# Kernel optimization log

Measured on AMD Instinct MI355X. Metric: run time of the kernel, lower is better.

Reference implementation:

```python
import jax, jax.numpy as jnp
import numpy as np

DIM = 1024
HEADS = 16
HEAD_DIM = 64
INNER = HEADS * HEAD_DIM
SCALE = HEAD_DIM ** -0.5


def setup_inputs() -> dict:
    key = jax.random.key(0)
    k1, k2, k3, k4 = jax.random.split(key, 4)
    x = jax.random.normal(k1, (4, 2048, DIM), dtype=jnp.float32)
    # nn.Linear(dim, 3*inner) without bias; weight stored [out, in], we keep [in, out]
    w_qkv = jax.random.normal(k2, (DIM, 3 * INNER), dtype=jnp.float32) * (DIM ** -0.5)
    w_proj = jax.random.normal(k3, (INNER, DIM), dtype=jnp.float32) * (INNER ** -0.5)
    b_proj = jax.random.normal(k4, (DIM,), dtype=jnp.float32) * 0.01
    return {"x": x, "w_qkv": w_qkv, "w_proj": w_proj, "b_proj": b_proj}


def reference(x, w_qkv, w_proj, b_proj):
    B, N, _ = x.shape
    qkv = x @ w_qkv                                   # [B,N,3*inner]
    qkv = qkv.reshape(B, N, 3, HEADS, HEAD_DIM)
    q = qkv[:, :, 0].transpose(0, 2, 1, 3)           # [B,H,N,D]
    k = qkv[:, :, 1].transpose(0, 2, 1, 3)
    v = qkv[:, :, 2].transpose(0, 2, 1, 3)
    attn = jnp.einsum("bhqd,bhkd->bhqk", q, k) * SCALE
    attn = jax.nn.softmax(attn, axis=-1)
    out = jnp.einsum("bhqk,bhkd->bhqd", attn, v)     # [B,H,N,D]
    out = out.transpose(0, 2, 1, 3).reshape(B, N, INNER)
    return out @ w_proj + b_proj
```

## Files before the change

### kernel.cpp

```cpp
#include <hip/hip_runtime.h>

typedef unsigned short u16;
typedef unsigned int   u32;
typedef __attribute__((ext_vector_type(2))) float    f32x2;
typedef __attribute__((ext_vector_type(4))) float    f32x4;
typedef __attribute__((ext_vector_type(8))) __bf16   bf16x8;
typedef __attribute__((ext_vector_type(8))) unsigned short u16x8;
typedef __attribute__((ext_vector_type(4))) unsigned short u16x4;
typedef __attribute__((ext_vector_type(4))) float    float4v;

#define MFMA16(a,b,c) __builtin_amdgcn_mfma_f32_16x16x32_bf16((a),(b),(c),0,0,0)
#define QSCALE 0.18033688011112042f

__device__ __forceinline__ u16 f2b(float f){
  union { float f; unsigned u; } v; v.f = f;
  return (u16)((v.u + 0x7fffu + ((v.u >> 16) & 1u)) >> 16);
}

__device__ __forceinline__ u32 cvt_pk_bf16(float lo, float hi){
  u32 r;
  asm("v_cvt_pk_bf16_f32 %0, %1, %2" : "=v"(r) : "v"(lo), "v"(hi));
  return r;
}

__device__ __forceinline__ float exp2_raw(float x){
  float r;
  asm("v_exp_f32 %0, %1" : "=v"(r) : "v"(x));
  return r;
}

__device__ __forceinline__ f32x2 lo2(f32x4 v){ return __builtin_shufflevector(v, v, 0, 1); }
__device__ __forceinline__ f32x2 hi2(f32x4 v){ return __builtin_shufflevector(v, v, 2, 3); }

__device__ __forceinline__ void gload_lds16(const void* g, void* l){
  __builtin_amdgcn_global_load_lds(
      (const __attribute__((address_space(1))) void*)g,
      (__attribute__((address_space(3))) void*)l, 16, 0, 0);
}

__global__ void cast_f32_bf16(const float* __restrict__ in, u16* __restrict__ out, int n4){
  int i = blockIdx.x * blockDim.x + threadIdx.x;
  int st = gridDim.x * blockDim.x;
  for (; i < n4; i += st){
    float4v v = ((const float4v*)in)[i];
    u16x4 o;
    o[0] = f2b(v[0]); o[1] = f2b(v[1]); o[2] = f2b(v[2]); o[3] = f2b(v[3]);
    ((u16x4*)out)[i] = o;
  }
}

__global__ void tcast(const float* __restrict__ src, u16* __restrict__ dst, int R, int C){
  __shared__ float tile[32][33];
  int tx = threadIdx.x, ty = threadIdx.y;
  int c0 = blockIdx.x * 32, r0 = blockIdx.y * 32;
  #pragma unroll
  for (int i = 0; i < 4; i++)
    tile[ty + i*8][tx] = src[(long)(r0 + ty + i*8) * C + c0 + tx];
  __syncthreads();
  #pragma unroll
  for (int i = 0; i < 4; i++)
    dst[(long)(c0 + ty + i*8) * R + r0 + tx] = f2b(tile[tx][ty + i*8]);
}

template<int MODE>
__global__ __launch_bounds__(512, 2) void gemm8(
    const u16* __restrict__ A, const u16* __restrict__ Bt,
    int M, int N, int K,
    float* __restrict__ outF, const float* __restrict__ bias,
    u16* __restrict__ qb, u16* __restrict__ kb, u16* __restrict__ vtb)
{
  extern __shared__ u16 lds[];
  u16* aL = lds;
  u16* bL = lds + 49152;

  const int t  = threadIdx.x;
  const int l  = t & 63, lr = l & 15, lg = l >> 4;
  const int w  = t >> 6;
  const int wm = w >> 2, wn = w & 3;
  const long mbase = (long)blockIdx.x * 256;
  const long nbase = (long)blockIdx.y * 128;

  const int xr0 = t >> 3;
  const int xc  = t & 7;
  const int xswz = (xc ^ (xr0 & 7)) << 3;

#define STG(F_) do { \
    const int T_ = (F_) >> 2, h_ = (F_) & 3, slot_ = T_ % 3; \
    if ((h_ & 1) == 0){ const int ah = h_ >> 1; \
      const u16* g_ = A + (mbase + ah*128 + xr0)*(long)K + T_*64 + xswz; \
      u16* d_ = aL + slot_*16384 + ah*8192 + t*8; \
      gload_lds16(g_, d_); \
      gload_lds16(g_ + 64*(long)K, d_ + 4096); \
    } else { const int bh_ = h_ >> 1; \
      const u16* g_ = Bt + (nbase + bh_*64 + xr0)*(long)K + T_*64 + xswz; \
      gload_lds16(g_, bL + slot_*8192 + bh_*4096 + t*8); } \
  } while(0)

#define VMCNT(n) asm volatile("s_waitcnt vmcnt(" #n ")" ::: "memory")
#define BAR() __builtin_amdgcn_s_barrier()

  f32x4 z = {0.f,0.f,0.f,0.f};
  f32x4 acc[8][2];
  #pragma unroll
  for (int a = 0; a < 8; a++){ acc[a][0] = z; acc[a][1] = z; }

  STG(0); STG(1); STG(2); STG(3);
  STG(4); STG(5); STG(6); STG(7);
  VMCNT(6);
  BAR();

  for (int T = 0; T < 16; ++T){
    const int abuf = (T % 3) * 16384;
    const int bbuf = (T % 3) * 8192;
    bf16x8 af[8], bf[2];

    #pragma unroll
    for (int i = 0; i < 8; i++){
      const int ra = wm*128 + i*16 + lr;
      af[i] = *(const bf16x8*)&aL[abuf + ra*64 + ((lg^(ra&7))<<3)];
    }
    #pragma unroll
    for (int j = 0; j < 2; j++){
      const int rb = wn*32 + j*16 + lr;
      bf[j] = *(const bf16x8*)&bL[bbuf + rb*64 + ((lg^(rb&7))<<3)];
    }
    if (T < 14){ STG(4*(T+2)); STG(4*(T+2)+1); }
    __builtin_amdgcn_s_setprio(1);
    #pragma unroll
    for (int i = 0; i < 8; i++){
      acc[i][0] = MFMA16(af[i], bf[0], acc[i][0]);
      acc[i][1] = MFMA16(af[i], bf[1], acc[i][1]);
    }
    __builtin_amdgcn_s_setprio(0);
    BAR();

    #pragma unroll
    for (int i = 0; i < 8; i++){
      const int ra = wm*128 + i*16 + lr;
      af[i] = *(const bf16x8*)&aL[abuf + ra*64 + (((4+lg)^(ra&7))<<3)];
    }
    #pragma unroll
    for (int j = 0; j < 2; j++){
      const int rb = wn*32 + j*16 + lr;
      bf[j] = *(const bf16x8*)&bL[bbuf + rb*64 + (((4+lg)^(rb&7))<<3)];
    }
    if (T < 14){ STG(4*(T+2)+2); STG(4*(T+2)+3); }
    if (T < 14){ VMCNT(6); } else if (T == 14){ VMCNT(0); }
    BAR();
    __builtin_amdgcn_s_setprio(1);
    #pragma unroll
    for (int i = 0; i < 8; i++){
      acc[i][0] = MFMA16(af[i], bf[0], acc[i][0]);
      acc[i][1] = MFMA16(af[i], bf[1], acc[i][1]);
    }
    __builtin_amdgcn_s_setprio(0);
    BAR();
  }
#undef STG
#undef VMCNT
#undef BAR

  if (MODE == 0){
    #pragma unroll
    for (int a = 0; a < 8; a++){
      #pragma unroll
      for (int j = 0; j < 2; j++){
        int col   = (int)nbase + wn*32 + j*16 + lr;
        int which = col >> 10;
        int h     = (col >> 6) & 15;
        int d     = col & 63;
        int m0    = (int)mbase + wm*128 + a*16 + lg*4;
        int b     = m0 >> 11, ns0 = m0 & 2047;
        int bh    = (b << 4) + h;
        if (which == 2){
          u16x4 pk;
          #pragma unroll
          for (int r = 0; r < 4; r++) pk[r] = f2b(acc[a][j][r]);
          *(u16x4*)&vtb[((long)bh*64 + d)*2048 + ns0] = pk;
        } else {
          u16* dst  = (which == 0) ? qb : kb;
          float scl = (which == 0) ? QSCALE : 1.0f;
          #pragma unroll
          for (int r = 0; r < 4; r++)
            dst[((long)bh * 2048 + ns0 + r) * 64 + d] = f2b(acc[a][j][r] * scl);
        }
      }
    }
  } else {
    #pragma unroll
    for (int a = 0; a < 8; a++){
      #pragma unroll
      for (int j = 0; j < 2; j++){
        int c = (int)nbase + wn*32 + j*16 + lr;
        float bv = bias[c];
        #pragma unroll
        for (int r = 0; r < 4; r++){
          int m = (int)mbase + wm*128 + a*16 + lg*4 + r;
          outF[(long)m * N + c] = acc[a][j][r] + bv;
        }
      }
    }
  }
}

__global__ __launch_bounds__(256, 2) void attn_fused(
    const u16* __restrict__ qb, const u16* __restrict__ kb,
    const u16* __restrict__ vtb, u16* __restrict__ ob)
{
  __shared__ u16 k_lds[2][64*64];
  __shared__ u16 vt_lds[2][64*64];
  const int t  = threadIdx.x;
  const int l  = t & 63, lr = l & 15, lg = l >> 4;
  const int w  = t >> 6;
  const int bid = blockIdx.x;
  const int vid = (bid & 7) * 128 + (bid >> 3);
  const int bh = vid >> 4, qt = vid & 15;
  const int qrow = qt*128 + w*32;
  const int h7 = lr & 7;

  const u16* Qp = qb + ((long)bh*2048 + qrow)*64;
  bf16x8 qfA0 = *(const bf16x8*)&Qp[lr*64 + lg*8];
  bf16x8 qfA1 = *(const bf16x8*)&Qp[lr*64 + 32 + lg*8];
  bf16x8 qfB0 = *(const bf16x8*)&Qp[(16+lr)*64 + lg*8];
  bf16x8 qfB1 = *(const bf16x8*)&Qp[(16+lr)*64 + 32 + lg*8];

  const int r1 = t >> 3;
  const int cx = ((t & 7) ^ (r1 & 7)) * 8;
  const u16* Kp = kb  + (long)bh*2048*64;
  const u16* Vt = vtb + (long)bh*64*2048;
  const int koff0 = r1*64 + cx,        koff1 = (r1+32)*64 + cx;
  const int voff0 = r1*2048 + cx,      voff1 = (r1+32)*2048 + cx;

#define STAGE(kv, buf) do { \
    gload_lds16(Kp + (long)(kv)*64 + koff0, &k_lds[buf][t*8]); \
    gload_lds16(Kp + (long)(kv)*64 + koff1, &k_lds[buf][2048 + t*8]); \
    gload_lds16(Vt + (kv) + voff0, &vt_lds[buf][t*8]); \
    gload_lds16(Vt + (kv) + voff1, &vt_lds[buf][2048 + t*8]); \
  } while(0)

  f32x4 z = {0.f,0.f,0.f,0.f};
  f32x4 oaccA[4] = {z,z,z,z}, oaccB[4] = {z,z,z,z};
  f32x2 sAacc = {0.f, 0.f}, sBacc = {0.f, 0.f};

  STAGE(0, 0);
  #pragma unroll 2
  for (int it = 0; it < 32; ++it){
    const int cur = it & 1;
    __syncthreads();
    if (it < 31) STAGE((it+1)*64, cur^1);

    const u16* kl = k_lds[cur];
    const u16* vl = vt_lds[cur];

    f32x4 stA[4], stB[4];
    __builtin_amdgcn_s_setprio(1);
    #pragma unroll
    for (int k4 = 0; k4 < 4; k4++){
      const int row = (k4*16 + lr)*64;
      bf16x8 kf0 = *(const bf16x8*)&kl[row + ((0+lg)^h7)*8];
      bf16x8 kf1 = *(const bf16x8*)&kl[row + ((4+lg)^h7)*8];
      stA[k4] = MFMA16(kf0, qfA0, z);
      stA[k4] = MFMA16(kf1, qfA1, stA[k4]);
      stB[k4] = MFMA16(kf0, qfB0, z);
      stB[k4] = MFMA16(kf1, qfB1, stB[k4]);
    }
    __builtin_amdgcn_s_setprio(0);

    u32 wvA[4][2], wvB[4][2];
    #pragma unroll
    for (int k4 = 0; k4 < 4; k4++){
      f32x2 e0 = lo2(stA[k4]), e1 = hi2(stA[k4]);
      e0[0] = exp2_raw(e0[0]); e0[1] = exp2_raw(e0[1]);
      e1[0] = exp2_raw(e1[0]); e1[1] = exp2_raw(e1[1]);
      sAacc += e0 + e1;
      wvA[k4][0] = cvt_pk_bf16(e0[0], e0[1]);
      wvA[k4][1] = cvt_pk_bf16(e1[0], e1[1]);
      f32x2 f0 = lo2(stB[k4]), f1 = hi2(stB[k4]);
      f0[0] = exp2_raw(f0[0]); f0[1] = exp2_raw(f0[1]);
      f1[0] = exp2_raw(f1[0]); f1[1] = exp2_raw(f1[1]);
      sBacc += f0 + f1;
      wvB[k4][0] = cvt_pk_bf16(f0[0], f0[1]);
      wvB[k4][1] = cvt_pk_bf16(f1[0], f1[1]);
    }

    union { u32 u[4]; bf16x8 v; } paA0, paA1, paB0, paB1;
    paA0.u[0]=wvA[0][0]; paA0.u[1]=wvA[0][1]; paA0.u[2]=wvA[1][0]; paA0.u[3]=wvA[1][1];
    paA1.u[0]=wvA[2][0]; paA1.u[1]=wvA[2][1]; paA1.u[2]=wvA[3][0]; paA1.u[3]=wvA[3][1];
    paB0.u[0]=wvB[0][0]; paB0.u[1]=wvB[0][1]; paB0.u[2]=wvB[1][0]; paB0.u[3]=wvB[1][1];
    paB1.u[0]=wvB[2][0]; paB1.u[1]=wvB[2][1]; paB1.u[2]=wvB[3][0]; paB1.u[3]=wvB[3][1];

    const int vhalf = (lg & 1) * 4;
    const int cA    = lg >> 1;
    #pragma unroll
    for (int nt = 0; nt < 4; nt++){
      const int rb = (nt*16 + lr)*64;
      u16x4 a0_ = *(const u16x4*)&vl[rb + ((cA     ^ h7)*8) + vhalf];
      u16x4 a1_ = *(const u16x4*)&vl[rb + (((cA+2) ^ h7)*8) + vhalf];
      u16x4 a2_ = *(const u16x4*)&vl[rb + (((cA+4) ^ h7)*8) + vhalf];
      u16x4 a3_ = *(const u16x4*)&vl[rb + (((cA+6) ^ h7)*8) + vhalf];
      u16x8 s0 = __builtin_shufflevector(a0_, a1_, 0,1,2,3,4,5,6,7);
      u16x8 s1 = __builtin_shufflevector(a2_, a3_, 0,1,2,3,4,5,6,7);
      __builtin_amdgcn_s_setprio(1);
      oaccA[nt] = MFMA16(paA0.v, *(bf16x8*)&s0, oaccA[nt]);
      oaccA[nt] = MFMA16(paA1.v, *(bf16x8*)&s1, oaccA[nt]);
      oaccB[nt] = MFMA16(paB0.v, *(bf16x8*)&s0, oaccB[nt]);
      oaccB[nt] = MFMA16(paB1.v, *(bf16x8*)&s1, oaccB[nt]);
      __builtin_amdgcn_s_setprio(0);
    }
  }
#undef STAGE

  float rsA = sAacc[0] + sAacc[1];
  rsA += __shfl_xor(rsA, 16, 64);
  rsA += __shfl_xor(rsA, 32, 64);
  float rsB = sBacc[0] + sBacc[1];
  rsB += __shfl_xor(rsB, 16, 64);
  rsB += __shfl_xor(rsB, 32, 64);
  float linvA = 1.0f / rsA, linvB = 1.0f / rsB;

  const int b = bh >> 4, h = bh & 15;
  #pragma unroll
  for (int r = 0; r < 4; r++){
    float lrA = __shfl(linvA, lg*4 + r, 64);
    float lrB = __shfl(linvB, lg*4 + r, 64);
    long mA = (long)b*2048 + qrow + lg*4 + r;
    long mB = mA + 16;
    #pragma unroll
    for (int nt = 0; nt < 4; nt++){
      ob[mA*1024 + h*64 + nt*16 + lr] = f2b(oaccA[nt][r] * lrA);
      ob[mB*1024 + h*64 + nt*16 + lr] = f2b(oaccB[nt][r] * lrB);
    }
  }
}

extern "C" void kernel_launch(void* const* d_in, const int* in_sizes, int n_in,
                              void* d_out, int out_size, void* d_ws, size_t ws_size,
                              hipStream_t stream)
{
  const float* x      = (const float*)d_in[0];
  const float* w_qkv  = (const float*)d_in[1];
  const float* w_proj = (const float*)d_in[2];
  const float* b_proj = (const float*)d_in[3];
  float* out = (float*)d_out;

  char* ws = (char*)d_ws;
  size_t off = 0;
  u16* xb     = (u16*)(ws + off);
  u16* obuf   = xb;
  off += (size_t)8192*1024*2;
  u16* wqkvt  = (u16*)(ws + off); off += (size_t)3072*1024*2;
  u16* wprojt = (u16*)(ws + off); off += (size_t)1024*1024*2;
  u16* qbuf   = (u16*)(ws + off); off += (size_t)64*2048*64*2;
  u16* kbuf   = (u16*)(ws + off); off += (size_t)64*2048*64*2;
  u16* vtb    = (u16*)(ws + off); off += (size_t)64*64*2048*2;

  hipFuncSetAttribute(reinterpret_cast<const void*>(&gemm8<0>),
                      hipFuncAttributeMaxDynamicSharedMemorySize, 147456);
  hipFuncSetAttribute(reinterpret_cast<const void*>(&gemm8<1>),
                      hipFuncAttributeMaxDynamicSharedMemorySize, 147456);

  cast_f32_bf16<<<2048, 256, 0, stream>>>(x, xb, (8192*1024)/4);
  tcast<<<dim3(96, 32), dim3(32, 8), 0, stream>>>(w_qkv, wqkvt, 1024, 3072);
  tcast<<<dim3(32, 32), dim3(32, 8), 0, stream>>>(w_proj, wprojt, 1024, 1024);

  gemm8<0><<<dim3(32, 24), 512, 147456, stream>>>(xb, wqkvt, 8192, 3072, 1024,
                                                  nullptr, nullptr, qbuf, kbuf, vtb);
  attn_fused<<<dim3(1024), 256, 0, stream>>>(qbuf, kbuf, vtb, obuf);
  gemm8<1><<<dim3(32, 8), 512, 147456, stream>>>(obuf, wprojt, 8192, 1024, 1024,
                                                 out, b_proj, nullptr, nullptr, nullptr);
}
```

Before: 188.8 us.

## Split GEMM K across warp pairs and enlarge attention query tile per wave

The GEMM now assigns each pair of waves the two K-halves of a 64-wide N slab, so each wave issues 32 MFMAs per tile with one barrier phase instead of two, and the partial sums are then combined through LDS. The attention kernel gives each wave 64 query rows instead of 32, halving the block count and reusing each K/V LDS fragment across four query groups. The aim is to cut LDS fragment reloads and barriers per MFMA. In exchange, register pressure rises sharply (acc[8][4] and oacc[4][4] plus st[4][4]), which may cause spills or lower occupancy, and the GEMM gains a serialized LDS reduction epilogue.

```diff
diff --git a/kernel.cpp b/kernel.cpp
--- a/kernel.cpp
+++ b/kernel.cpp
@@ -76,7 +76,7 @@
   const int t  = threadIdx.x;
   const int l  = t & 63, lr = l & 15, lg = l >> 4;
   const int w  = t >> 6;
-  const int wm = w >> 2, wn = w & 3;
+  const int wm = w >> 2, wn = (w >> 1) & 1, wk = w & 1;
   const long mbase = (long)blockIdx.x * 256;
   const long nbase = (long)blockIdx.y * 128;
 
@@ -100,9 +100,13 @@
 #define BAR() __builtin_amdgcn_s_barrier()
 
   f32x4 z = {0.f,0.f,0.f,0.f};
-  f32x4 acc[8][2];
-  #pragma unroll
-  for (int a = 0; a < 8; a++){ acc[a][0] = z; acc[a][1] = z; }
+  f32x4 acc[8][4];
+  #pragma unroll
+  for (int a = 0; a < 8; a++)
+    #pragma unroll
+    for (int j = 0; j < 4; j++) acc[a][j] = z;
+
+  const int kc = wk*4;
 
   STG(0); STG(1); STG(2); STG(3);
   STG(4); STG(5); STG(6); STG(7);
@@ -112,47 +116,31 @@
   for (int T = 0; T < 16; ++T){
     const int abuf = (T % 3) * 16384;
     const int bbuf = (T % 3) * 8192;
-    bf16x8 af[8], bf[2];
-
+    bf16x8 afi[8], bfj[4];
+
+    #pragma unroll
+    for (int j = 0; j < 4; j++){
+      const int rb = wn*64 + j*16 + lr;
+      bfj[j] = *(const bf16x8*)&bL[bbuf + rb*64 + (((kc+lg)^(rb&7))<<3)];
+    }
     #pragma unroll
     for (int i = 0; i < 8; i++){
       const int ra = wm*128 + i*16 + lr;
-      af[i] = *(const bf16x8*)&aL[abuf + ra*64 + ((lg^(ra&7))<<3)];
-    }
-    #pragma unroll
-    for (int j = 0; j < 2; j++){
-      const int rb = wn*32 + j*16 + lr;
-      bf[j] = *(const bf16x8*)&bL[bbuf + rb*64 + ((lg^(rb&7))<<3)];
-    }
-    if (T < 14){ STG(4*(T+2)); STG(4*(T+2)+1); }
-    __builtin_amdgcn_s_setprio(1);
-    #pragma unroll
-    for (int i = 0; i < 8; i++){
-      acc[i][0] = MFMA16(af[i], bf[0], acc[i][0]);
-      acc[i][1] = MFMA16(af[i], bf[1], acc[i][1]);
-    }
-    __builtin_amdgcn_s_setprio(0);
-    BAR();
-
-    #pragma unroll
-    for (int i = 0; i < 8; i++){
-      const int ra = wm*128 + i*16 + lr;
-      af[i] = *(const bf16x8*)&aL[abuf + ra*64 + (((4+lg)^(ra&7))<<3)];
-    }
-    #pragma unroll
-    for (int j = 0; j < 2; j++){
-      const int rb = wn*32 + j*16 + lr;
-      bf[j] = *(const bf16x8*)&bL[bbuf + rb*64 + (((4+lg)^(rb&7))<<3)];
-    }
-    if (T < 14){ STG(4*(T+2)+2); STG(4*(T+2)+3); }
-    if (T < 14){ VMCNT(6); } else if (T == 14){ VMCNT(0); }
+      afi[i] = *(const bf16x8*)&aL[abuf + ra*64 + (((kc+lg)^(ra&7))<<3)];
+    }
+    if (T < 14){
+      STG(4*(T+2)); STG(4*(T+2)+1); STG(4*(T+2)+2); STG(4*(T+2)+3);
+      VMCNT(6);
+    } else if (T == 14){
+      VMCNT(0);
+    }
     BAR();
     __builtin_amdgcn_s_setprio(1);
     #pragma unroll
-    for (int i = 0; i < 8; i++){
-      acc[i][0] = MFMA16(af[i], bf[0], acc[i][0]);
-      acc[i][1] = MFMA16(af[i], bf[1], acc[i][1]);
-    }
+    for (int i = 0; i < 8; i++)
+      #pragma unroll
+      for (int j = 0; j < 4; j++)
+        acc[i][j] = MFMA16(afi[i], bfj[j], acc[i][j]);
     __builtin_amdgcn_s_setprio(0);
     BAR();
   }
@@ -160,29 +148,51 @@
 #undef VMCNT
 #undef BAR
 
+  if (wk){
+    #pragma unroll
+    for (int a = 0; a < 8; a++){
+      f32x4 t0 = acc[a][0]; acc[a][0] = acc[a][2]; acc[a][2] = t0;
+      f32x4 t1 = acc[a][1]; acc[a][1] = acc[a][3]; acc[a][3] = t1;
+    }
+  }
+  f32x4* red = (f32x4*)lds;
+  const int pb = (wm*2 + wn)*2;
+  const int wme = pb + (1 - wk);
+  const int rme = pb + wk;
+  #pragma unroll
+  for (int a = 0; a < 8; a++){
+    red[(wme*2 + 0)*64 + l] = acc[a][2];
+    red[(wme*2 + 1)*64 + l] = acc[a][3];
+    __builtin_amdgcn_s_barrier();
+    acc[a][0] += red[(rme*2 + 0)*64 + l];
+    acc[a][1] += red[(rme*2 + 1)*64 + l];
+    __builtin_amdgcn_s_barrier();
+  }
+
   if (MODE == 0){
     #pragma unroll
     for (int a = 0; a < 8; a++){
       #pragma unroll
-      for (int j = 0; j < 2; j++){
-        int col   = (int)nbase + wn*32 + j*16 + lr;
+      for (int jj = 0; jj < 2; jj++){
+        int col   = (int)nbase + wn*64 + (wk*2 + jj)*16 + lr;
         int which = col >> 10;
         int h     = (col >> 6) & 15;
         int d     = col & 63;
         int m0    = (int)mbase + wm*128 + a*16 + lg*4;
         int b     = m0 >> 11, ns0 = m0 & 2047;
         int bh    = (b << 4) + h;
+        f32x4 v   = (jj == 0) ? acc[a][0] : acc[a][1];
         if (which == 2){
           u16x4 pk;
           #pragma unroll
-          for (int r = 0; r < 4; r++) pk[r] = f2b(acc[a][j][r]);
+          for (int r = 0; r < 4; r++) pk[r] = f2b(v[r]);
           *(u16x4*)&vtb[((long)bh*64 + d)*2048 + ns0] = pk;
         } else {
           u16* dst  = (which == 0) ? qb : kb;
           float scl = (which == 0) ? QSCALE : 1.0f;
           #pragma unroll
           for (int r = 0; r < 4; r++)
-            dst[((long)bh * 2048 + ns0 + r) * 64 + d] = f2b(acc[a][j][r] * scl);
+            dst[((long)bh * 2048 + ns0 + r) * 64 + d] = f2b(v[r] * scl);
         }
       }
     }
@@ -190,13 +200,14 @@
     #pragma unroll
     for (int a = 0; a < 8; a++){
       #pragma unroll
-      for (int j = 0; j < 2; j++){
-        int c = (int)nbase + wn*32 + j*16 + lr;
+      for (int jj = 0; jj < 2; jj++){
+        int c = (int)nbase + wn*64 + (wk*2 + jj)*16 + lr;
         float bv = bias[c];
+        f32x4 v = (jj == 0) ? acc[a][0] : acc[a][1];
         #pragma unroll
         for (int r = 0; r < 4; r++){
           int m = (int)mbase + wm*128 + a*16 + lg*4 + r;
-          outF[(long)m * N + c] = acc[a][j][r] + bv;
+          outF[(long)m * N + c] = v[r] + bv;
         }
       }
     }
@@ -213,16 +224,18 @@
   const int l  = t & 63, lr = l & 15, lg = l >> 4;
   const int w  = t >> 6;
   const int bid = blockIdx.x;
-  const int vid = (bid & 7) * 128 + (bid >> 3);
-  const int bh = vid >> 4, qt = vid & 15;
-  const int qrow = qt*128 + w*32;
+  const int vid = (bid & 7) * 64 + (bid >> 3);
+  const int bh = vid >> 3, qt = vid & 7;
+  const int qrow = qt*256 + w*64;
   const int h7 = lr & 7;
 
   const u16* Qp = qb + ((long)bh*2048 + qrow)*64;
-  bf16x8 qfA0 = *(const bf16x8*)&Qp[lr*64 + lg*8];
-  bf16x8 qfA1 = *(const bf16x8*)&Qp[lr*64 + 32 + lg*8];
-  bf16x8 qfB0 = *(const bf16x8*)&Qp[(16+lr)*64 + lg*8];
-  bf16x8 qfB1 = *(const bf16x8*)&Qp[(16+lr)*64 + 32 + lg*8];
+  bf16x8 qf0[4], qf1[4];
+  #pragma unroll
+  for (int g = 0; g < 4; g++){
+    qf0[g] = *(const bf16x8*)&Qp[(g*16+lr)*64 + lg*8];
+    qf1[g] = *(const bf16x8*)&Qp[(g*16+lr)*64 + 32 + lg*8];
+  }
 
   const int r1 = t >> 3;
   const int cx = ((t & 7) ^ (r1 & 7)) * 8;
@@ -239,11 +252,16 @@
   } while(0)
 
   f32x4 z = {0.f,0.f,0.f,0.f};
-  f32x4 oaccA[4] = {z,z,z,z}, oaccB[4] = {z,z,z,z};
-  f32x2 sAacc = {0.f, 0.f}, sBacc = {0.f, 0.f};
+  f32x4 oacc[4][4];
+  f32x2 sacc[4];
+  #pragma unroll
+  for (int g = 0; g < 4; g++){
+    sacc[g] = (f32x2){0.f, 0.f};
+    #pragma unroll
+    for (int nt = 0; nt < 4; nt++) oacc[g][nt] = z;
+  }
 
   STAGE(0, 0);
-  #pragma unroll 2
   for (int it = 0; it < 32; ++it){
     const int cur = it & 1;
     __syncthreads();
@@ -252,42 +270,39 @@
     const u16* kl = k_lds[cur];
     const u16* vl = vt_lds[cur];
 
-    f32x4 stA[4], stB[4];
+    f32x4 st[4][4];
     __builtin_amdgcn_s_setprio(1);
     #pragma unroll
     for (int k4 = 0; k4 < 4; k4++){
       const int row = (k4*16 + lr)*64;
       bf16x8 kf0 = *(const bf16x8*)&kl[row + ((0+lg)^h7)*8];
       bf16x8 kf1 = *(const bf16x8*)&kl[row + ((4+lg)^h7)*8];
-      stA[k4] = MFMA16(kf0, qfA0, z);
-      stA[k4] = MFMA16(kf1, qfA1, stA[k4]);
-      stB[k4] = MFMA16(kf0, qfB0, z);
-      stB[k4] = MFMA16(kf1, qfB1, stB[k4]);
+      #pragma unroll
+      for (int g = 0; g < 4; g++){
+        st[g][k4] = MFMA16(kf0, qf0[g], z);
+        st[g][k4] = MFMA16(kf1, qf1[g], st[g][k4]);
+      }
     }
     __builtin_amdgcn_s_setprio(0);
 
-    u32 wvA[4][2], wvB[4][2];
-    #pragma unroll
-    for (int k4 = 0; k4 < 4; k4++){
-      f32x2 e0 = lo2(stA[k4]), e1 = hi2(stA[k4]);
-      e0[0] = exp2_raw(e0[0]); e0[1] = exp2_raw(e0[1]);
-      e1[0] = exp2_raw(e1[0]); e1[1] = exp2_raw(e1[1]);
-      sAacc += e0 + e1;
-      wvA[k4][0] = cvt_pk_bf16(e0[0], e0[1]);
-      wvA[k4][1] = cvt_pk_bf16(e1[0], e1[1]);
-      f32x2 f0 = lo2(stB[k4]), f1 = hi2(stB[k4]);
-      f0[0] = exp2_raw(f0[0]); f0[1] = exp2_raw(f0[1]);
-      f1[0] = exp2_raw(f1[0]); f1[1] = exp2_raw(f1[1]);
-      sBacc += f0 + f1;
-      wvB[k4][0] = cvt_pk_bf16(f0[0], f0[1]);
-      wvB[k4][1] = cvt_pk_bf16(f1[0], f1[1]);
-    }
-
-    union { u32 u[4]; bf16x8 v; } paA0, paA1, paB0, paB1;
-    paA0.u[0]=wvA[0][0]; paA0.u[1]=wvA[0][1]; paA0.u[2]=wvA[1][0]; paA0.u[3]=wvA[1][1];
-    paA1.u[0]=wvA[2][0]; paA1.u[1]=wvA[2][1]; paA1.u[2]=wvA[3][0]; paA1.u[3]=wvA[3][1];
-    paB0.u[0]=wvB[0][0]; paB0.u[1]=wvB[0][1]; paB0.u[2]=wvB[1][0]; paB0.u[3]=wvB[1][1];
-    paB1.u[0]=wvB[2][0]; paB1.u[1]=wvB[2][1]; paB1.u[2]=wvB[3][0]; paB1.u[3]=wvB[3][1];
+    bf16x8 pa0[4], pa1[4];
+    #pragma unroll
+    for (int g = 0; g < 4; g++){
+      u32 wv[4][2];
+      #pragma unroll
+      for (int k4 = 0; k4 < 4; k4++){
+        f32x2 e0 = lo2(st[g][k4]), e1 = hi2(st[g][k4]);
+        e0[0] = exp2_raw(e0[0]); e0[1] = exp2_raw(e0[1]);
+        e1[0] = exp2_raw(e1[0]); e1[1] = exp2_raw(e1[1]);
+        sacc[g] += e0 + e1;
+        wv[k4][0] = cvt_pk_bf16(e0[0], e0[1]);
+        wv[k4][1] = cvt_pk_bf16(e1[0], e1[1]);
+      }
+      union { u32 u[4]; bf16x8 v; } p0, p1;
+      p0.u[0]=wv[0][0]; p0.u[1]=wv[0][1]; p0.u[2]=wv[1][0]; p0.u[3]=wv[1][1];
+      p1.u[0]=wv[2][0]; p1.u[1]=wv[2][1]; p1.u[2]=wv[3][0]; p1.u[3]=wv[3][1];
+      pa0[g] = p0.v; pa1[g] = p1.v;
+    }
 
     const int vhalf = (lg & 1) * 4;
     const int cA    = lg >> 1;
@@ -301,34 +316,30 @@
       u16x8 s0 = __builtin_shufflevector(a0_, a1_, 0,1,2,3,4,5,6,7);
       u16x8 s1 = __builtin_shufflevector(a2_, a3_, 0,1,2,3,4,5,6,7);
       __builtin_amdgcn_s_setprio(1);
-      oaccA[nt] = MFMA16(paA0.v, *(bf16x8*)&s0, oaccA[nt]);
-      oaccA[nt] = MFMA16(paA1.v, *(bf16x8*)&s1, oaccA[nt]);
-      oaccB[nt] = MFMA16(paB0.v, *(bf16x8*)&s0, oaccB[nt]);
-      oaccB[nt] = MFMA16(paB1.v, *(bf16x8*)&s1, oaccB[nt]);
+      #pragma unroll
+      for (int g = 0; g < 4; g++){
+        oacc[g][nt] = MFMA16(pa0[g], *(bf16x8*)&s0, oacc[g][nt]);
+        oacc[g][nt] = MFMA16(pa1[g], *(bf16x8*)&s1, oacc[g][nt]);
+      }
       __builtin_amdgcn_s_setprio(0);
     }
   }
 #undef STAGE
 
-  float rsA = sAacc[0] + sAacc[1];
-  rsA += __shfl_xor(rsA, 16, 64);
-  rsA += __shfl_xor(rsA, 32, 64);
-  float rsB = sBacc[0] + sBacc[1];
-  rsB += __shfl_xor(rsB, 16, 64);
-  rsB += __shfl_xor(rsB, 32, 64);
-  float linvA = 1.0f / rsA, linvB = 1.0f / rsB;
-
   const int b = bh >> 4, h = bh & 15;
   #pragma unroll
-  for (int r = 0; r < 4; r++){
-    float lrA = __shfl(linvA, lg*4 + r, 64);
-    float lrB = __shfl(linvB, lg*4 + r, 64);
-    long mA = (long)b*2048 + qrow + lg*4 + r;
-    long mB = mA + 16;
-    #pragma unroll
-    for (int nt = 0; nt < 4; nt++){
-      ob[mA*1024 + h*64 + nt*16 + lr] = f2b(oaccA[nt][r] * lrA);
-      ob[mB*1024 + h*64 + nt*16 + lr] = f2b(oaccB[nt][r] * lrB);
+  for (int g = 0; g < 4; g++){
+    float rs = sacc[g][0] + sacc[g][1];
+    rs += __shfl_xor(rs, 16, 64);
+    rs += __shfl_xor(rs, 32, 64);
+    float linv = 1.0f / rs;
+    #pragma unroll
+    for (int r = 0; r < 4; r++){
+      float lrr = __shfl(linv, lg*4 + r, 64);
+      long m = (long)b*2048 + qrow + g*16 + lg*4 + r;
+      #pragma unroll
+      for (int nt = 0; nt < 4; nt++)
+        ob[m*1024 + h*64 + nt*16 + lr] = f2b(oacc[g][nt][r] * lrr);
     }
   }
 }
@@ -365,7 +376,7 @@
 
   gemm8<0><<<dim3(32, 24), 512, 147456, stream>>>(xb, wqkvt, 8192, 3072, 1024,
                                                   nullptr, nullptr, qbuf, kbuf, vtb);
-  attn_fused<<<dim3(1024), 256, 0, stream>>>(qbuf, kbuf, vtb, obuf);
+  attn_fused<<<dim3(512), 256, 0, stream>>>(qbuf, kbuf, vtb, obuf);
   gemm8<1><<<dim3(32, 8), 512, 147456, stream>>>(obuf, wprojt, 8192, 1024, 1024,
                                                  out, b_proj, nullptr, nullptr, nullptr);
 }
```

Measured after the change: 180.9 us. -4.2%, faster.
